# Performance work log

Measured on AMD Instinct MI355X. Metric: run time of the kernel, lower is better.

## Reference

```python
import jax, jax.numpy as jnp
import numpy as np

T, U, I, B, K = 64, 142, 4500, 16384, 10


def setup_inputs() -> dict:
    key = jax.random.key(0)
    k1, k2, k3, k4, k5, k6 = jax.random.split(key, 6)
    q = jax.random.uniform(k1, (T, U, I), dtype=jnp.float32, minval=0.01, maxval=5.0)
    miss = jax.random.uniform(k2, (T, U, I)) < 0.3
    qos_tensor = jnp.where(miss, 0.0, q)
    # user_avg exactly as in __init__: sum over items / count of rated items (clamped >= 1)
    cnt = jnp.clip((qos_tensor > 0).sum(axis=2).astype(jnp.float32), 1.0, None)
    user_avg = qos_tensor.sum(axis=2) / cnt  # [T, U]
    # time-aggregated similarity: random symmetric matrix in [-1, 1]
    s = jax.random.uniform(k3, (U, U), dtype=jnp.float32, minval=-1.0, maxval=1.0)
    user_sim_agg = 0.5 * (s + s.T)
    user_id = jax.random.randint(k4, (B,), 0, U)
    item_id = jax.random.randint(k5, (B,), 0, I)
    time_id = jax.random.randint(k6, (B,), 0, T)
    return {
        "qos_tensor": qos_tensor,
        "user_avg": user_avg,
        "user_sim_agg": user_sim_agg,
        "user_id": user_id,
        "item_id": item_id,
        "time_id": time_id,
        "top_k": K,
    }


def reference(qos_tensor, user_avg, user_sim_agg, user_id, item_id, time_id, top_k):
    num_users = qos_tensor.shape[1]
    avg_u = user_avg[time_id, user_id]                      # [B]
    sim_u = user_sim_agg[user_id]                           # [B, U]
    # ratings of every user for (time_id, item_id): column gather, [B, U]
    u_idx = jnp.arange(num_users)[None, :]
    item_col = qos_tensor[time_id[:, None], u_idx, item_id[:, None]]
    item_rated = item_col > 0                               # [B, U]
    sim_m = jnp.where(item_rated, sim_u, 0.0)
    top_sim, top_user = jax.lax.top_k(sim_m, top_k)         # [B, K]
    top_sim = top_sim / (top_sim.sum(axis=1, keepdims=True) + 1e-8)
    top_sim = jnp.nan_to_num(top_sim)
    # neighbor ratings and neighbor averages
    r_vs = qos_tensor[time_id[:, None], top_user, item_id[:, None]]  # [B, K]
    avg_v = user_avg[time_id[:, None], top_user]                     # [B, K]
    pred = avg_u + (top_sim * (r_vs - avg_v)).sum(axis=1)            # [B]
    return pred
```

## Files before the change

kernel.cpp:

```cpp
#include <hip/hip_runtime.h>
#include <math.h>

#define T_DIM 64
#define U_DIM 142
#define I_DIM 4500
#define B_DIM 16384
#define K_TOP 10

#define NWPC  5
#define NCH   18
#define MASK_INTS ((size_t)T_DIM * I_DIM * NWPC)
#define WS_BYTES  (MASK_INTS * sizeof(unsigned))

__global__ __launch_bounds__(256) void build_mask(
    const float* __restrict__ qos,
    unsigned*    __restrict__ mask)
{
    const int lane = threadIdx.x & 63;
    const int gw   = blockIdx.x * 4 + (threadIdx.x >> 6);
    const int w    = gw % NWPC;
    const int tc   = gw / NWPC;
    const int c    = tc % NCH;
    const int t    = tc / NCH;

    const int i0 = c * 256 + lane * 4;
    if (i0 + 3 >= I_DIM) return;

    const int v0 = w * 32;
    const int nv = (w == 4) ? (U_DIM - 128) : 32;

    const float* p = qos + ((size_t)t * U_DIM + v0) * I_DIM + i0;
    unsigned m0 = 0, m1 = 0, m2 = 0, m3 = 0;
#pragma unroll 4
    for (int k = 0; k < nv; ++k, p += I_DIM) {
        const float4 q = *(const float4*)p;
        const unsigned bit = 1u << ((v0 + k) & 31);
        if (q.x > 0.0f) m0 |= bit;
        if (q.y > 0.0f) m1 |= bit;
        if (q.z > 0.0f) m2 |= bit;
        if (q.w > 0.0f) m3 |= bit;
    }
    unsigned* mp = mask + ((size_t)t * I_DIM + i0) * NWPC + w;
    mp[0 * NWPC] = m0;
    mp[1 * NWPC] = m1;
    mp[2 * NWPC] = m2;
    mp[3 * NWPC] = m3;
}

__global__ __launch_bounds__(256) void ucf_select(
    const float*    __restrict__ qos,
    const float*    __restrict__ user_avg,
    const float*    __restrict__ user_sim,
    const int*      __restrict__ user_id,
    const int*      __restrict__ item_id,
    const int*      __restrict__ time_id,
    const unsigned* __restrict__ mask,
    float*          __restrict__ out)
{
    const int lane = threadIdx.x & 63;
    const int wid  = threadIdx.x >> 6;
    const int b    = blockIdx.x * 4 + wid;
    if (b >= B_DIM) return;

    const int u = user_id[b];
    const int i = item_id[b];
    const int t = time_id[b];

    const unsigned* mp = mask + ((size_t)t * I_DIM + i) * NWPC;
    const unsigned mw = (lane < NWPC) ? mp[lane] : 0u;

    const float* srow = user_sim + (size_t)u * U_DIM;
    const float* arow = user_avg + (size_t)t * U_DIM;

    const unsigned wA = __shfl(mw, lane >> 5, 64);
    const unsigned wB = __shfl(mw, 2 + (lane >> 5), 64);
    const unsigned wC = __shfl(mw, 4, 64);
    const unsigned bitm = 1u << (lane & 31);

    float val0 = (wA & bitm) ? srow[lane] : 0.0f;
    float val1 = (wB & bitm) ? srow[lane + 64] : 0.0f;
    float val2 = -INFINITY;
    const bool has2 = (lane + 128) < U_DIM;
    if (has2) val2 = (wC & bitm) ? srow[lane + 128] : 0.0f;

    float ssum = 0.0f;
    float wv[K_TOP];
    int   wk[K_TOP];
#pragma unroll
    for (int k = 0; k < K_TOP; ++k) {
        float mv = val0; int mk = lane;
        if (val1 > mv) { mv = val1; mk = lane + 64; }
        if (val2 > mv) { mv = val2; mk = lane + 128; }
#pragma unroll
        for (int off = 32; off > 0; off >>= 1) {
            const float ov = __shfl_xor(mv, off, 64);
            const int   ok = __shfl_xor(mk, off, 64);
            if (ov > mv || (ov == mv && ok < mk)) { mv = ov; mk = ok; }
        }
        wv[k] = mv;
        wk[k] = mk;
        ssum += mv;
        const int sl = mk >> 6;
        const int wl = mk & 63;
        if (wl == lane) {
            if (sl == 0)      val0 = -INFINITY;
            else if (sl == 1) val1 = -INFINITY;
            else              val2 = -INFINITY;
        }
    }

    float myval = 0.0f; int myv = -1;
#pragma unroll
    for (int k = 0; k < K_TOP; ++k)
        if (lane == k) { myv = wk[k]; myval = wv[k]; }

    float c = 0.0f;
    if (myv >= 0) {
        const float rv = qos[((size_t)t * U_DIM + (size_t)myv) * I_DIM + i];
        const float av = arow[myv];
        c = myval * (rv - av);
    }

    float wsum = 0.0f;
#pragma unroll
    for (int k = 0; k < K_TOP; ++k)
        wsum += __shfl(c, k, 64);

    if (lane == 0)
        out[b] = arow[u] + wsum / (ssum + 1e-8f);
}

__global__ __launch_bounds__(256) void ucf_kernel(
    const float* __restrict__ qos,
    const float* __restrict__ user_avg,
    const float* __restrict__ user_sim,
    const int*   __restrict__ user_id,
    const int*   __restrict__ item_id,
    const int*   __restrict__ time_id,
    float*       __restrict__ out)
{
    const int lane = threadIdx.x & 63;
    const int wid  = threadIdx.x >> 6;
    const int b    = blockIdx.x * 4 + wid;
    if (b >= B_DIM) return;

    const int u = user_id[b];
    const int i = item_id[b];
    const int t = time_id[b];

    const float* qcol = qos + ((size_t)t * U_DIM) * (size_t)I_DIM + i;
    const float* srow = user_sim + (size_t)u * U_DIM;
    const float* arow = user_avg + (size_t)t * U_DIM;

    float val[3];
    float con[3];
#pragma unroll
    for (int j = 0; j < 3; ++j) {
        const int v = lane + j * 64;
        float sv = -INFINITY;
        float cv = 0.0f;
        if (v < U_DIM) {
            const float rv = qcol[(size_t)v * I_DIM];
            const float av = arow[v];
            const float s  = srow[v];
            sv = (rv > 0.0f) ? s : 0.0f;
            cv = sv * (rv - av);
        }
        val[j] = sv;
        con[j] = cv;
    }

    float ssum = 0.0f, wsum = 0.0f;
#pragma unroll
    for (int k = 0; k < K_TOP; ++k) {
        float mv = val[0]; float mc = con[0]; int mk = lane;
        if (val[1] > mv) { mv = val[1]; mc = con[1]; mk = lane + 64; }
        if (val[2] > mv) { mv = val[2]; mc = con[2]; mk = lane + 128; }
#pragma unroll
        for (int off = 32; off > 0; off >>= 1) {
            const float ov = __shfl_xor(mv, off, 64);
            const float oc = __shfl_xor(mc, off, 64);
            const int   ok = __shfl_xor(mk, off, 64);
            if (ov > mv || (ov == mv && ok < mk)) { mv = ov; mc = oc; mk = ok; }
        }
        ssum += mv;
        wsum += mc;
        if ((mk & 63) == lane) {
            const int slot = mk >> 6;
            if (slot == 0)      val[0] = -INFINITY;
            else if (slot == 1) val[1] = -INFINITY;
            else                val[2] = -INFINITY;
        }
    }

    if (lane == 0) {
        out[b] = arow[u] + wsum / (ssum + 1e-8f);
    }
}

extern "C" void kernel_launch(void* const* d_in, const int* in_sizes, int n_in,
                              void* d_out, int out_size, void* d_ws, size_t ws_size,
                              hipStream_t stream) {
    const float* qos  = (const float*)d_in[0];
    const float* uavg = (const float*)d_in[1];
    const float* usim = (const float*)d_in[2];
    const int*   uid  = (const int*)d_in[3];
    const int*   iid  = (const int*)d_in[4];
    const int*   tid  = (const int*)d_in[5];
    float* out = (float*)d_out;

    if (d_ws != nullptr && ws_size >= WS_BYTES) {
        unsigned* mask = (unsigned*)d_ws;
        build_mask<<<dim3(T_DIM * NCH * NWPC / 4), dim3(256), 0, stream>>>(qos, mask);
        ucf_select<<<dim3(B_DIM / 4), dim3(256), 0, stream>>>(
            qos, uavg, usim, uid, iid, tid, mask, out);
    } else {
        ucf_kernel<<<dim3(B_DIM / 4), dim3(256), 0, stream>>>(
            qos, uavg, usim, uid, iid, tid, out);
    }
}
```

Baseline: 269.5 us.

## Transpose bitmask layout to pack items per user word

The precomputed rating mask now packs 32 consecutive items into one word per user, indexed by (time, item-block, user), instead of packing users into words per (time, item). In the build kernel each lane now handles one user row and issues eight independent float4 loads over 128 contiguous bytes, which gives more loads in flight than the old serial loop over users. In the select kernel each lane reads its own mask words directly, so the shuffles are no longer needed. The cost is that each select query reads more mask bytes, and the build's loads are strided across lanes, so coalescing relies on cache lines.

```diff
diff --git a/kernel.cpp b/kernel.cpp
--- a/kernel.cpp
+++ b/kernel.cpp
@@ -7,54 +7,55 @@
 #define B_DIM 16384
 #define K_TOP 10
 
-#define NWPC  5
-#define NCH   18
-#define MASK_INTS ((size_t)T_DIM * I_DIM * NWPC)
-#define WS_BYTES  (MASK_INTS * sizeof(unsigned))
-
-__global__ __launch_bounds__(256) void build_mask(
+#define NIW   141
+#define PADV  144
+#define MASK_WORDS ((size_t)T_DIM * NIW * PADV)
+#define WS_BYTES   (MASK_WORDS * sizeof(unsigned))
+
+__global__ __launch_bounds__(256) void build_mask2(
     const float* __restrict__ qos,
-    unsigned*    __restrict__ mask)
+    unsigned*    __restrict__ mask2)
 {
     const int lane = threadIdx.x & 63;
     const int gw   = blockIdx.x * 4 + (threadIdx.x >> 6);
-    const int w    = gw % NWPC;
-    const int tc   = gw / NWPC;
-    const int c    = tc % NCH;
-    const int t    = tc / NCH;
-
-    const int i0 = c * 256 + lane * 4;
-    if (i0 + 3 >= I_DIM) return;
-
-    const int v0 = w * 32;
-    const int nv = (w == 4) ? (U_DIM - 128) : 32;
-
-    const float* p = qos + ((size_t)t * U_DIM + v0) * I_DIM + i0;
-    unsigned m0 = 0, m1 = 0, m2 = 0, m3 = 0;
-#pragma unroll 4
-    for (int k = 0; k < nv; ++k, p += I_DIM) {
-        const float4 q = *(const float4*)p;
-        const unsigned bit = 1u << ((v0 + k) & 31);
-        if (q.x > 0.0f) m0 |= bit;
-        if (q.y > 0.0f) m1 |= bit;
-        if (q.z > 0.0f) m2 |= bit;
-        if (q.w > 0.0f) m3 |= bit;
-    }
-    unsigned* mp = mask + ((size_t)t * I_DIM + i0) * NWPC + w;
-    mp[0 * NWPC] = m0;
-    mp[1 * NWPC] = m1;
-    mp[2 * NWPC] = m2;
-    mp[3 * NWPC] = m3;
-}
-
-__global__ __launch_bounds__(256) void ucf_select(
+    const int iw   = gw % NIW;
+    const int t    = gw / NIW;
+    const int i0   = iw * 32;
+    const int nf4  = (iw == NIW - 1) ? 5 : 8;
+    unsigned* mout = mask2 + ((size_t)t * NIW + iw) * PADV;
+
+#pragma unroll
+    for (int r = 0; r < 3; ++r) {
+        const int v = lane + 64 * r;
+        if (v < U_DIM) {
+            const float* p = qos + ((size_t)t * U_DIM + v) * I_DIM + i0;
+            float4 q[8];
+#pragma unroll
+            for (int m = 0; m < 8; ++m)
+                if (m < nf4) q[m] = *(const float4*)(p + m * 4);
+            unsigned word = 0;
+#pragma unroll
+            for (int m = 0; m < 8; ++m) {
+                if (m < nf4) {
+                    if (q[m].x > 0.0f) word |= 1u << (4 * m + 0);
+                    if (q[m].y > 0.0f) word |= 1u << (4 * m + 1);
+                    if (q[m].z > 0.0f) word |= 1u << (4 * m + 2);
+                    if (q[m].w > 0.0f) word |= 1u << (4 * m + 3);
+                }
+            }
+            mout[v] = word;
+        }
+    }
+}
+
+__global__ __launch_bounds__(256) void ucf_select2(
     const float*    __restrict__ qos,
     const float*    __restrict__ user_avg,
     const float*    __restrict__ user_sim,
     const int*      __restrict__ user_id,
     const int*      __restrict__ item_id,
     const int*      __restrict__ time_id,
-    const unsigned* __restrict__ mask,
+    const unsigned* __restrict__ mask2,
     float*          __restrict__ out)
 {
     const int lane = threadIdx.x & 63;
@@ -66,22 +67,21 @@
     const int i = item_id[b];
     const int t = time_id[b];
 
-    const unsigned* mp = mask + ((size_t)t * I_DIM + i) * NWPC;
-    const unsigned mw = (lane < NWPC) ? mp[lane] : 0u;
+    const unsigned* mp = mask2 + ((size_t)t * NIW + (i >> 5)) * PADV;
+    const unsigned bitm = 1u << (i & 31);
+
+    const unsigned w0 = mp[lane];
+    const unsigned w1 = mp[lane + 64];
+    const bool has2 = (lane + 128) < U_DIM;
+    const unsigned w2 = has2 ? mp[lane + 128] : 0u;
 
     const float* srow = user_sim + (size_t)u * U_DIM;
     const float* arow = user_avg + (size_t)t * U_DIM;
 
-    const unsigned wA = __shfl(mw, lane >> 5, 64);
-    const unsigned wB = __shfl(mw, 2 + (lane >> 5), 64);
-    const unsigned wC = __shfl(mw, 4, 64);
-    const unsigned bitm = 1u << (lane & 31);
-
-    float val0 = (wA & bitm) ? srow[lane] : 0.0f;
-    float val1 = (wB & bitm) ? srow[lane + 64] : 0.0f;
+    float val0 = (w0 & bitm) ? srow[lane] : 0.0f;
+    float val1 = (w1 & bitm) ? srow[lane + 64] : 0.0f;
     float val2 = -INFINITY;
-    const bool has2 = (lane + 128) < U_DIM;
-    if (has2) val2 = (wC & bitm) ? srow[lane + 128] : 0.0f;
+    if (has2) val2 = (w2 & bitm) ? srow[lane + 128] : 0.0f;
 
     float ssum = 0.0f;
     float wv[K_TOP];
@@ -210,10 +210,10 @@
     float* out = (float*)d_out;
 
     if (d_ws != nullptr && ws_size >= WS_BYTES) {
-        unsigned* mask = (unsigned*)d_ws;
-        build_mask<<<dim3(T_DIM * NCH * NWPC / 4), dim3(256), 0, stream>>>(qos, mask);
-        ucf_select<<<dim3(B_DIM / 4), dim3(256), 0, stream>>>(
-            qos, uavg, usim, uid, iid, tid, mask, out);
+        unsigned* mask2 = (unsigned*)d_ws;
+        build_mask2<<<dim3(T_DIM * NIW / 4), dim3(256), 0, stream>>>(qos, mask2);
+        ucf_select2<<<dim3(B_DIM / 4), dim3(256), 0, stream>>>(
+            qos, uavg, usim, uid, iid, tid, mask2, out);
     } else {
         ucf_kernel<<<dim3(B_DIM / 4), dim3(256), 0, stream>>>(
             qos, uavg, usim, uid, iid, tid, out);
```

After: 274.5 us. No clear change (+1.8%).
